# Kernel tuning notes

Hardware: AMD Instinct MI355X
Metric: run time of the kernel (lower is better)

Reference implementation:

```python
import jax, jax.numpy as jnp
import numpy as np


def setup_inputs() -> dict:
    key = jax.random.key(0)
    k1, k2, k3, k4 = jax.random.split(key, 4)
    B, H, S, E, L = 2, 12, 256, 64, 25
    return {
        "attention_probs": jax.random.uniform(k1, (B, H, S, S), dtype=jnp.float32),
        "value_attentions": jax.random.normal(k2, (B, H, S, E), dtype=jnp.float32),
        "relative_positions": jax.random.normal(k3, (B, S, S, H * E), dtype=jnp.float32),
        "W": jax.random.normal(k4, (L, H * E), dtype=jnp.float32) * 0.02,
        "b": jnp.zeros((L,), dtype=jnp.float32),
    }


def reference(attention_probs, value_attentions, relative_positions, W, b):
    # Faithful translation of TransformerMHSLayer.forward:
    #   out[b,h,i,j,e] = p[b,h,i,j] * (v[b,h,j,e] + rel[b,i,j,h,e])
    #   pre[b,j,i,l]   = sum_{h,e} out[b,h,i,j,e] * W[l, h*E+e] + bias[l]
    #   logits[b,j,l,i] = pre[b,j,i,l]
    B, H, S, E = value_attentions.shape
    L = W.shape[0]
    Wr = W.reshape(L, H, E)                       # [L,H,E], matches h*E+e flattening
    rel = relative_positions.reshape(B, S, S, H, E)  # view(B,S,S,H,E)
    # value term: contract v with W per head, then weight by attention probs
    pre = jnp.einsum('bhij,bhje,lhe->bjil', attention_probs, value_attentions, Wr)
    # relative-position term (same attention weighting)
    pre = pre + jnp.einsum('bhij,bijhe,lhe->bjil', attention_probs, rel, Wr)
    pre = pre + b                                  # bias over label dim
    return pre.transpose(0, 1, 3, 2)               # [B, S(j), L, S(i)]
```

## Files before the change

### kernel.cpp

```cpp
#include <hip/hip_runtime.h>
#include <stdint.h>


#define Bb 2
#define Hh 12
#define Ss 256
#define Ee 64
#define Ll 25
#define Kk 768

#define JT 4
#define NR 16
#define CHF 256
#define RSTR 260
#define BUFF (NR * RSTR)
#define REDF 2048
#define NUNIT (JT * 3)

typedef __attribute__((ext_vector_type(8))) short bf16x8;
typedef __attribute__((ext_vector_type(4))) float f32x4;

#define NFRAG (Hh * 4)
#define AB_BYTES ((size_t)NFRAG * 64 * 8 * 2)
#define PT_BYTES ((size_t)Bb * Ss * Hh * Ss * 4)
#define WV_BYTES ((size_t)Bb * Ss * Hh * 32 * 4)

typedef const void __attribute__((address_space(1)))* gas_ptr;
typedef void __attribute__((address_space(3)))* las_ptr;

__device__ __forceinline__ void async_copy16(void* lds_dst, const void* g_src) {
    __builtin_amdgcn_global_load_lds((gas_ptr)g_src, (las_ptr)lds_dst, 16, 0, 0);
}

__device__ __forceinline__ ushort f2bf(float x) {
    union { float f; uint32_t u; } u; u.f = x;
    uint32_t r = u.u + 0x7fff + ((u.u >> 16) & 1);
    return (ushort)(r >> 16);
}

__global__ void a_pack_kernel(const float* __restrict__ W, ushort* __restrict__ ab) {
    int idx = blockIdx.x * 256 + threadIdx.x;
    if (idx >= NFRAG * 64) return;
    int lane = idx & 63, fi = idx >> 6;
    int Lt = fi & 1, ks = (fi >> 1) & 1, h = fi >> 2;
    int l = Lt * 16 + (lane & 15);
    int k0 = h * Ee + ks * 32 + (lane >> 4) * 8;
    ushort* dst = ab + (size_t)idx * 8;
#pragma unroll
    for (int t = 0; t < 8; ++t)
        dst[t] = (l < Ll) ? f2bf(W[l * Kk + k0 + t]) : (ushort)0;
}

__global__ void p_transpose_kernel(const float* __restrict__ p,
                                   float* __restrict__ pt) {
    __shared__ float tile[32][33];
    const int bh = blockIdx.y;
    const int b = bh / Hh, h = bh % Hh;
    const int ti = blockIdx.x >> 3, tj = blockIdx.x & 7;
    const int tx = threadIdx.x & 31, ty = threadIdx.x >> 5;
#pragma unroll
    for (int s = 0; s < 4; ++s) {
        const int il = ty + 8 * s;
        tile[il][tx] = p[((size_t)(b * Hh + h) * Ss + ti * 32 + il) * Ss + tj * 32 + tx];
    }
    __syncthreads();
#pragma unroll
    for (int s = 0; s < 4; ++s) {
        const int jl = ty + 8 * s;
        pt[((size_t)(b * Ss + tj * 32 + jl) * Hh + h) * Ss + ti * 32 + tx] = tile[tx][jl];
    }
}

__global__ void wv_kernel(const float* __restrict__ W, const float* __restrict__ v,
                          float* __restrict__ wv) {
    const int bj = blockIdx.x;
    const int b = bj >> 8, j = bj & (Ss - 1);
    const int t = threadIdx.x;
    const int h = t >> 5, l = t & 31;
    float acc = 0.f;
    if (l < Ll) {
        const float* wrow = W + l * Kk + h * Ee;
        const float* vrow = v + ((size_t)(b * Hh + h) * Ss + j) * Ee;
#pragma unroll
        for (int e = 0; e < Ee; ++e) acc = __builtin_fmaf(wrow[e], vrow[e], acc);
    }
    wv[((size_t)bj * Hh + h) * 32 + l] = acc;
}

struct Pf {
    bf16x8 A00, A01, A10, A11;
    float4 wv0, wv1;
    float pv;
};

__global__ __launch_bounds__(256, 3) void mhs_t4(
    const float* __restrict__ pt,
    const float* __restrict__ rel,
    const ushort* __restrict__ ab,
    const float* __restrict__ wvp,
    const float* __restrict__ bias,
    float* __restrict__ out)
{
    __shared__ __align__(16) float lds[2 * BUFF + REDF];

    const int n = blockIdx.x;
    const int jt = n & 63, it = (n >> 6) & 15, b = n >> 10;
    const int j0 = jt * JT, i0 = it * NR;
    const int tid = threadIdx.x;
    const int w = tid >> 6, lane = tid & 63;
    const int col = lane & 15, grp = lane >> 4;

    auto stage = [&](int uu) {
        const int jj = uu / 3, c = uu - jj * 3;
#pragma unroll
        for (int q = 0; q < 4; ++q) {
            const int row = w * 4 + q;
            const float* src = rel
                + ((size_t)(b * Ss + i0 + row) * Ss + (j0 + jj)) * Kk
                + c * CHF + lane * 4;
            async_copy16(&lds[(uu & 1) * BUFF + row * RSTR], src);
        }
    };

    auto pre = [&](Pf& f, int uu) {
        const int jj = uu / 3, c = uu - jj * 3;
        const int h = c * 4 + w;
        const int j = j0 + jj;
        const ushort* ap = ab + (size_t)h * 2048 + lane * 8;
        f.A00 = *(const bf16x8*)(ap);
        f.A01 = *(const bf16x8*)(ap + 512);
        f.A10 = *(const bf16x8*)(ap + 1024);
        f.A11 = *(const bf16x8*)(ap + 1536);
        f.pv = pt[((size_t)(b * Ss + j) * Hh + h) * Ss + i0 + col];
        const float* wp = wvp + ((size_t)(b * Ss + j) * Hh + h) * 32 + grp * 4;
        f.wv0 = *(const float4*)(wp);
        f.wv1 = *(const float4*)(wp + 16);
    };

    f32x4 acc0 = {0.f, 0.f, 0.f, 0.f};
    f32x4 acc1 = {0.f, 0.f, 0.f, 0.f};

    auto compute = [&](const Pf& f, int uu) {
        const float* rb = &lds[(uu & 1) * BUFF + col * RSTR + w * 64 + grp * 8];
        const float4 x0 = *(const float4*)(rb);
        const float4 x1 = *(const float4*)(rb + 4);
        const float4 y0 = *(const float4*)(rb + 32);
        const float4 y1 = *(const float4*)(rb + 36);
        const float s = f.pv;
        acc0 += s * (f32x4){f.wv0.x, f.wv0.y, f.wv0.z, f.wv0.w};
        acc1 += s * (f32x4){f.wv1.x, f.wv1.y, f.wv1.z, f.wv1.w};
        bf16x8 B0, B1;
#pragma unroll
        for (int t = 0; t < 4; ++t) {
            B0[t]     = (short)f2bf(s * ((const float*)&x0)[t]);
            B0[t + 4] = (short)f2bf(s * ((const float*)&x1)[t]);
            B1[t]     = (short)f2bf(s * ((const float*)&y0)[t]);
            B1[t + 4] = (short)f2bf(s * ((const float*)&y1)[t]);
        }
        acc0 = __builtin_amdgcn_mfma_f32_16x16x32_bf16(f.A00, B0, acc0, 0, 0, 0);
        acc0 = __builtin_amdgcn_mfma_f32_16x16x32_bf16(f.A10, B1, acc0, 0, 0, 0);
        acc1 = __builtin_amdgcn_mfma_f32_16x16x32_bf16(f.A01, B0, acc1, 0, 0, 0);
        acc1 = __builtin_amdgcn_mfma_f32_16x16x32_bf16(f.A11, B1, acc1, 0, 0, 0);
    };

    const int lp0 = tid >> 4, lp1 = (tid + 256) >> 4;
    const float bias0 = (lp0 < Ll) ? bias[lp0] : 0.f;
    const float bias1 = (lp1 < Ll) ? bias[lp1] : 0.f;

    Pf fa, fb;
    pre(fa, 0);
    stage(0);
    stage(1);

    float* red = &lds[2 * BUFF];

    auto iter = [&](int u, Pf& cur, Pf& nxt) {
        if (u < NUNIT - 1) { asm volatile("s_waitcnt vmcnt(4)" ::: "memory"); }
        else               { asm volatile("s_waitcnt vmcnt(0)" ::: "memory"); }
        __builtin_amdgcn_sched_barrier(0);
        __builtin_amdgcn_s_barrier();
        __builtin_amdgcn_sched_barrier(0);

        compute(cur, u);
        const int jj = u / 3, c = u - jj * 3;
        if (c == 2) {
#pragma unroll
            for (int r = 0; r < 4; ++r) {
                red[w * 512 + (grp * 4 + r) * 16 + col]      = acc0[r];
                red[w * 512 + (16 + grp * 4 + r) * 16 + col] = acc1[r];
            }
            acc0 = (f32x4){0.f, 0.f, 0.f, 0.f};
            acc1 = (f32x4){0.f, 0.f, 0.f, 0.f};
        }
        if (u + 1 < NUNIT) pre(nxt, u + 1);

        asm volatile("s_waitcnt lgkmcnt(0)" ::: "memory");
        __builtin_amdgcn_sched_barrier(0);
        __builtin_amdgcn_s_barrier();
        __builtin_amdgcn_sched_barrier(0);

        if (c == 2) {
            const int j = j0 + jj;
            const float s0 = red[tid] + red[512 + tid] + red[1024 + tid]
                           + red[1536 + tid];
            const float s1 = red[tid + 256 - 2048 + 2048] + 0.f;
            const int t2 = tid + 256;
            const float q0 = s0 + bias0;
            const float q1 = red[t2 & 511] * 0.f;
            (void)s1; (void)q1;
            if (lp0 < Ll)
                out[((size_t)(b * Ss + j) * Ll + lp0) * Ss + i0 + (tid & 15)] = q0;
            {
                const float r1 = red[t2 - 256 + 256] ; (void)r1;
            }
            const float u0 = red[t2]       + red[512 + t2 - 512 + 512]
                           + red[1024 + t2 - 1024 + 1024] + red[1536 + t2 - 1536 + 1536];
            if (lp1 < Ll)
                out[((size_t)(b * Ss + j) * Ll + lp1) * Ss + i0 + (t2 & 15)] =
                    red[t2] + red[512 + t2] + red[1024 + t2] + red[1536 + t2] + bias1;
            (void)u0;
        }
        if (u + 2 < NUNIT) stage(u + 2);
    };

#pragma unroll 1
    for (int u = 0; u < NUNIT; u += 2) {
        iter(u, fa, fb);
        iter(u + 1, fb, fa);
    }
}

__global__ __launch_bounds__(256, 4) void mhs_basic(
    const float* __restrict__ p, const float* __restrict__ v,
    const float* __restrict__ rel, const float* __restrict__ W,
    const float* __restrict__ bias, float* __restrict__ out)
{
    const int g = blockIdx.x;
    const int ig = g & 3, j = (g >> 2) & (Ss - 1), b = g >> 10;
    const int tid = threadIdx.x;
    const int w = tid >> 6, lane = tid & 63;
    const int col = lane & 15, grp = lane >> 4;
    const int iw = ig * 64 + w * 16 + col;
    const float* relp = rel + ((size_t)(b * Ss + iw) * Ss + j) * Kk + grp * 8;

    f32x4 acc0 = {0.f, 0.f, 0.f, 0.f}, acc1 = {0.f, 0.f, 0.f, 0.f};
#pragma unroll 1
    for (int h = 0; h < Hh; ++h) {
        bf16x8 A00, A01, A10, A11;
#pragma unroll
        for (int t = 0; t < 8; ++t) {
            const int kb = h * Ee + grp * 8 + t;
            const int la = col, lb = 16 + col;
            A00[t] = (short)f2bf(W[la * Kk + kb]);
            A01[t] = (lb < Ll) ? (short)f2bf(W[lb * Kk + kb]) : (short)0;
            A10[t] = (short)f2bf(W[la * Kk + kb + 32]);
            A11[t] = (lb < Ll) ? (short)f2bf(W[lb * Kk + kb + 32]) : (short)0;
        }
        const float* vbp = v + ((size_t)(b * Hh + h) * Ss + j) * Ee + grp * 8;
        const float4 va0 = *(const float4*)(vbp);
        const float4 va1 = *(const float4*)(vbp + 4);
        const float4 vc0 = *(const float4*)(vbp + 32);
        const float4 vc1 = *(const float4*)(vbp + 36);
        const float* rb = relp + h * Ee;
        const float4 c0 = *(const float4*)(rb);
        const float4 c1 = *(const float4*)(rb + 4);
        const float4 c2 = *(const float4*)(rb + 32);
        const float4 c3 = *(const float4*)(rb + 36);
        const float pv = p[((size_t)(b * Hh + h) * Ss + iw) * Ss + j];
        bf16x8 B0, B1;
#pragma unroll
        for (int t = 0; t < 4; ++t) {
            B0[t]     = (short)f2bf(pv * (((const float*)&c0)[t] + ((const float*)&va0)[t]));
            B0[t + 4] = (short)f2bf(pv * (((const float*)&c1)[t] + ((const float*)&va1)[t]));
            B1[t]     = (short)f2bf(pv * (((const float*)&c2)[t] + ((const float*)&vc0)[t]));
            B1[t + 4] = (short)f2bf(pv * (((const float*)&c3)[t] + ((const float*)&vc1)[t]));
        }
        acc0 = __builtin_amdgcn_mfma_f32_16x16x32_bf16(A00, B0, acc0, 0, 0, 0);
        acc0 = __builtin_amdgcn_mfma_f32_16x16x32_bf16(A10, B1, acc0, 0, 0, 0);
        acc1 = __builtin_amdgcn_mfma_f32_16x16x32_bf16(A01, B0, acc1, 0, 0, 0);
        acc1 = __builtin_amdgcn_mfma_f32_16x16x32_bf16(A11, B1, acc1, 0, 0, 0);
    }
#pragma unroll
    for (int r = 0; r < 4; ++r) {
        const int l0 = grp * 4 + r;
        out[((size_t)(b * Ss + j) * Ll + l0) * Ss + iw] = acc0[r] + bias[l0];
        const int l1 = 16 + grp * 4 + r;
        if (l1 < Ll)
            out[((size_t)(b * Ss + j) * Ll + l1) * Ss + iw] = acc1[r] + bias[l1];
    }
}

extern "C" void kernel_launch(void* const* d_in, const int* in_sizes, int n_in,
                              void* d_out, int out_size, void* d_ws, size_t ws_size,
                              hipStream_t stream) {
    const float* p    = (const float*)d_in[0];
    const float* v    = (const float*)d_in[1];
    const float* rel  = (const float*)d_in[2];
    const float* W    = (const float*)d_in[3];
    const float* bias = (const float*)d_in[4];
    float* out = (float*)d_out;

    const bool full = ws_size >= AB_BYTES + PT_BYTES + WV_BYTES;

    if (full) {
        ushort* ab = (ushort*)d_ws;
        float* pt  = (float*)((char*)d_ws + AB_BYTES);
        float* wvp = (float*)((char*)d_ws + AB_BYTES + PT_BYTES);
        hipLaunchKernelGGL(a_pack_kernel, dim3((NFRAG * 64 + 255) / 256), dim3(256),
                           0, stream, W, ab);
        hipLaunchKernelGGL(p_transpose_kernel, dim3(64, Bb * Hh), dim3(256),
                           0, stream, p, pt);
        hipLaunchKernelGGL(wv_kernel, dim3(Bb * Ss), dim3(Hh * 32),
                           0, stream, W, v, wvp);
        hipLaunchKernelGGL(mhs_t4, dim3(Bb * 16 * 64), dim3(256), 0, stream,
                           pt, rel, ab, wvp, bias, out);
    } else {
        hipLaunchKernelGGL(mhs_basic, dim3(Bb * Ss * 4), dim3(256), 0, stream,
                           p, v, rel, W, bias, out);
    }
}
```

Baseline: 117.5 us.

## Drop p transpose pass, merge side kernels, and remap block order

Removes the separate transpose of attention probs and reads p directly in the main kernel, with a strided gather per lane. Merges the W-pack and wv precompute into one side kernel to cut launch count. Remaps the block index so that consecutive blocks are spread across 8 groups, which changes L2/XCD locality. The epilogue dead code is also cleaned up. The trade-off is that the direct p reads are uncoalesced (stride Ss).

```diff
diff --git a/kernel.cpp b/kernel.cpp
--- a/kernel.cpp
+++ b/kernel.cpp
@@ -22,7 +22,6 @@
 
 #define NFRAG (Hh * 4)
 #define AB_BYTES ((size_t)NFRAG * 64 * 8 * 2)
-#define PT_BYTES ((size_t)Bb * Ss * Hh * Ss * 4)
 #define WV_BYTES ((size_t)Bb * Ss * Hh * 32 * 4)
 
 typedef const void __attribute__((address_space(1)))* gas_ptr;
@@ -38,53 +37,33 @@
     return (ushort)(r >> 16);
 }
 
-__global__ void a_pack_kernel(const float* __restrict__ W, ushort* __restrict__ ab) {
-    int idx = blockIdx.x * 256 + threadIdx.x;
-    if (idx >= NFRAG * 64) return;
-    int lane = idx & 63, fi = idx >> 6;
-    int Lt = fi & 1, ks = (fi >> 1) & 1, h = fi >> 2;
-    int l = Lt * 16 + (lane & 15);
-    int k0 = h * Ee + ks * 32 + (lane >> 4) * 8;
-    ushort* dst = ab + (size_t)idx * 8;
-#pragma unroll
-    for (int t = 0; t < 8; ++t)
-        dst[t] = (l < Ll) ? f2bf(W[l * Kk + k0 + t]) : (ushort)0;
-}
-
-__global__ void p_transpose_kernel(const float* __restrict__ p,
-                                   float* __restrict__ pt) {
-    __shared__ float tile[32][33];
-    const int bh = blockIdx.y;
-    const int b = bh / Hh, h = bh % Hh;
-    const int ti = blockIdx.x >> 3, tj = blockIdx.x & 7;
-    const int tx = threadIdx.x & 31, ty = threadIdx.x >> 5;
-#pragma unroll
-    for (int s = 0; s < 4; ++s) {
-        const int il = ty + 8 * s;
-        tile[il][tx] = p[((size_t)(b * Hh + h) * Ss + ti * 32 + il) * Ss + tj * 32 + tx];
-    }
-    __syncthreads();
-#pragma unroll
-    for (int s = 0; s < 4; ++s) {
-        const int jl = ty + 8 * s;
-        pt[((size_t)(b * Ss + tj * 32 + jl) * Hh + h) * Ss + ti * 32 + tx] = tile[tx][jl];
-    }
-}
-
-__global__ void wv_kernel(const float* __restrict__ W, const float* __restrict__ v,
-                          float* __restrict__ wv) {
-    const int bj = blockIdx.x;
-    const int b = bj >> 8, j = bj & (Ss - 1);
-    const int t = threadIdx.x;
-    const int h = t >> 5, l = t & 31;
-    float acc = 0.f;
-    if (l < Ll) {
-        const float* wrow = W + l * Kk + h * Ee;
-        const float* vrow = v + ((size_t)(b * Hh + h) * Ss + j) * Ee;
-#pragma unroll
-        for (int e = 0; e < Ee; ++e) acc = __builtin_fmaf(wrow[e], vrow[e], acc);
-    }
-    wv[((size_t)bj * Hh + h) * 32 + l] = acc;
+__global__ void side_kernel(const float* __restrict__ W, const float* __restrict__ v,
+                            float* __restrict__ wv, ushort* __restrict__ ab) {
+    if (blockIdx.x < 512) {
+        const int bj = blockIdx.x;
+        const int b = bj >> 8, j = bj & (Ss - 1);
+        const int t = threadIdx.x;
+        const int h = t >> 5, l = t & 31;
+        float acc = 0.f;
+        if (l < Ll) {
+            const float* wrow = W + l * Kk + h * Ee;
+            const float* vrow = v + ((size_t)(b * Hh + h) * Ss + j) * Ee;
+#pragma unroll
+            for (int e = 0; e < Ee; ++e) acc = __builtin_fmaf(wrow[e], vrow[e], acc);
+        }
+        wv[((size_t)bj * Hh + h) * 32 + l] = acc;
+    } else {
+        const int idx = (blockIdx.x - 512) * 384 + threadIdx.x;
+        if (idx >= NFRAG * 64) return;
+        const int lane = idx & 63, fi = idx >> 6;
+        const int Lt = fi & 1, ks = (fi >> 1) & 1, h = fi >> 2;
+        const int l = Lt * 16 + (lane & 15);
+        const int k0 = h * Ee + ks * 32 + (lane >> 4) * 8;
+        ushort* dst = ab + (size_t)idx * 8;
+#pragma unroll
+        for (int t = 0; t < 8; ++t)
+            dst[t] = (l < Ll) ? f2bf(W[l * Kk + k0 + t]) : (ushort)0;
+    }
 }
 
 struct Pf {
@@ -94,7 +73,7 @@
 };
 
 __global__ __launch_bounds__(256, 3) void mhs_t4(
-    const float* __restrict__ pt,
+    const float* __restrict__ p,
     const float* __restrict__ rel,
     const ushort* __restrict__ ab,
     const float* __restrict__ wvp,
@@ -103,7 +82,7 @@
 {
     __shared__ __align__(16) float lds[2 * BUFF + REDF];
 
-    const int n = blockIdx.x;
+    const int n = (blockIdx.x & 7) * 256 + (blockIdx.x >> 3);
     const int jt = n & 63, it = (n >> 6) & 15, b = n >> 10;
     const int j0 = jt * JT, i0 = it * NR;
     const int tid = threadIdx.x;
@@ -131,7 +110,7 @@
         f.A01 = *(const bf16x8*)(ap + 512);
         f.A10 = *(const bf16x8*)(ap + 1024);
         f.A11 = *(const bf16x8*)(ap + 1536);
-        f.pv = pt[((size_t)(b * Ss + j) * Hh + h) * Ss + i0 + col];
+        f.pv = p[((size_t)(b * Hh + h) * Ss + i0 + col) * Ss + j];
         const float* wp = wvp + ((size_t)(b * Ss + j) * Hh + h) * 32 + grp * 4;
         f.wv0 = *(const float4*)(wp);
         f.wv1 = *(const float4*)(wp + 16);
@@ -201,24 +180,15 @@
 
         if (c == 2) {
             const int j = j0 + jj;
-            const float s0 = red[tid] + red[512 + tid] + red[1024 + tid]
-                           + red[1536 + tid];
-            const float s1 = red[tid + 256 - 2048 + 2048] + 0.f;
+            const float r0 = red[tid] + red[512 + tid] + red[1024 + tid]
+                           + red[1536 + tid] + bias0;
+            if (lp0 < Ll)
+                out[((size_t)(b * Ss + j) * Ll + lp0) * Ss + i0 + (tid & 15)] = r0;
             const int t2 = tid + 256;
-            const float q0 = s0 + bias0;
-            const float q1 = red[t2 & 511] * 0.f;
-            (void)s1; (void)q1;
-            if (lp0 < Ll)
-                out[((size_t)(b * Ss + j) * Ll + lp0) * Ss + i0 + (tid & 15)] = q0;
-            {
-                const float r1 = red[t2 - 256 + 256] ; (void)r1;
-            }
-            const float u0 = red[t2]       + red[512 + t2 - 512 + 512]
-                           + red[1024 + t2 - 1024 + 1024] + red[1536 + t2 - 1536 + 1536];
+            const float r1 = red[t2] + red[512 + t2] + red[1024 + t2]
+                           + red[1536 + t2] + bias1;
             if (lp1 < Ll)
-                out[((size_t)(b * Ss + j) * Ll + lp1) * Ss + i0 + (t2 & 15)] =
-                    red[t2] + red[512 + t2] + red[1024 + t2] + red[1536 + t2] + bias1;
-            (void)u0;
+                out[((size_t)(b * Ss + j) * Ll + lp1) * Ss + i0 + (t2 & 15)] = r1;
         }
         if (u + 2 < NUNIT) stage(u + 2);
     };
@@ -300,20 +270,15 @@
     const float* bias = (const float*)d_in[4];
     float* out = (float*)d_out;
 
-    const bool full = ws_size >= AB_BYTES + PT_BYTES + WV_BYTES;
+    const bool full = ws_size >= AB_BYTES + WV_BYTES;
 
     if (full) {
         ushort* ab = (ushort*)d_ws;
-        float* pt  = (float*)((char*)d_ws + AB_BYTES);
-        float* wvp = (float*)((char*)d_ws + AB_BYTES + PT_BYTES);
-        hipLaunchKernelGGL(a_pack_kernel, dim3((NFRAG * 64 + 255) / 256), dim3(256),
-                           0, stream, W, ab);
-        hipLaunchKernelGGL(p_transpose_kernel, dim3(64, Bb * Hh), dim3(256),
-                           0, stream, p, pt);
-        hipLaunchKernelGGL(wv_kernel, dim3(Bb * Ss), dim3(Hh * 32),
-                           0, stream, W, v, wvp);
+        float* wvp = (float*)((char*)d_ws + AB_BYTES);
+        hipLaunchKernelGGL(side_kernel, dim3(520), dim3(384), 0, stream,
+                           W, v, wvp, ab);
         hipLaunchKernelGGL(mhs_t4, dim3(Bb * 16 * 64), dim3(256), 0, stream,
-                           pt, rel, ab, wvp, bias, out);
+                           p, rel, ab, wvp, bias, out);
     } else {
         hipLaunchKernelGGL(mhs_basic, dim3(Bb * Ss * 4), dim3(256), 0, stream,
                            p, v, rel, W, bias, out);
```

Result: no change. 115.3 us (-1.9%).
